# Kernel optimization log

Measured on AMD Instinct MI355X. Metric: run time of the kernel, lower is better.

Reference implementation:

```python
import jax, jax.numpy as jnp
import numpy as np

N, E, F, H, C, K = 50000, 1600000, 256, 6, 16, 40
NEG_SLOPE = 0.2  # PyG GATConv default
EPS = 1e-16


def _gat_layer(x, src, dst, W, a_s, a_d, b, heads, out_ch, concat):
    # linear transform per head: [N, heads, out_ch]
    h = (x @ W).reshape(N, heads, out_ch)
    # per-node attention logits
    al_s = jnp.einsum('nhc,hc->nh', h, a_s)  # source term
    al_d = jnp.einsum('nhc,hc->nh', h, a_d)  # destination term
    # edge-wise score + segment softmax over incoming edges of each dst node
    e = jax.nn.leaky_relu(al_s[src] + al_d[dst], NEG_SLOPE)  # [E', heads]
    m = jax.ops.segment_max(e, dst, num_segments=N)
    ex = jnp.exp(e - m[dst])
    denom = jax.ops.segment_sum(ex, dst, num_segments=N)
    alpha = ex / (denom[dst] + EPS)  # [E', heads]
    # weighted scatter-add aggregation
    out = jax.ops.segment_sum(h[src] * alpha[:, :, None], dst, num_segments=N)
    out = out.reshape(N, heads * out_ch) if concat else out.mean(axis=1)
    return out + b


def setup_inputs() -> dict:
    key = jax.random.key(0)
    ks = jax.random.split(key, 16)
    s = 0.05
    inp = {
        'x': jax.random.normal(ks[0], (N, F), dtype=jnp.float32),
        'edge_index': jax.random.randint(ks[1], (2, E), 0, N, dtype=jnp.int64 if jax.config.jax_enable_x64 else jnp.int32),
        'W1': jax.random.normal(ks[2], (F, H * C), dtype=jnp.float32) * s,
        'a1_s': jax.random.normal(ks[3], (H, C), dtype=jnp.float32) * s,
        'a1_d': jax.random.normal(ks[4], (H, C), dtype=jnp.float32) * s,
        'b1': jnp.zeros((H * C,), dtype=jnp.float32),
        'W2': jax.random.normal(ks[5], (H * C, H * C), dtype=jnp.float32) * s,
        'a2_s': jax.random.normal(ks[6], (H, C), dtype=jnp.float32) * s,
        'a2_d': jax.random.normal(ks[7], (H, C), dtype=jnp.float32) * s,
        'b2': jnp.zeros((H * C,), dtype=jnp.float32),
        'W3': jax.random.normal(ks[8], (H * C, H * C), dtype=jnp.float32) * s,
        'a3_s': jax.random.normal(ks[9], (H, C), dtype=jnp.float32) * s,
        'a3_d': jax.random.normal(ks[10], (H, C), dtype=jnp.float32) * s,
        'b3': jnp.zeros((H * C,), dtype=jnp.float32),
        'W4': jax.random.normal(ks[11], (H * C, K), dtype=jnp.float32) * s,
        'a4_s': jax.random.normal(ks[12], (1, K), dtype=jnp.float32) * s,
        'a4_d': jax.random.normal(ks[13], (1, K), dtype=jnp.float32) * s,
        'b4': jnp.zeros((K,), dtype=jnp.float32),
    }
    return inp


def reference(x, edge_index, W1, a1_s, a1_d, b1, W2, a2_s, a2_d, b2,
              W3, a3_s, a3_d, b3, W4, a4_s, a4_d, b4):
    # PyG GATConv adds self-loops by default
    loops = jnp.arange(N, dtype=edge_index.dtype)
    src = jnp.concatenate([edge_index[0], loops])
    dst = jnp.concatenate([edge_index[1], loops])
    # dropout is identity at eval time
    h = jax.nn.relu(_gat_layer(x, src, dst, W1, a1_s, a1_d, b1, H, C, True))
    h = jax.nn.relu(_gat_layer(h, src, dst, W2, a2_s, a2_d, b2, H, C, True))
    h = jax.nn.relu(_gat_layer(h, src, dst, W3, a3_s, a3_d, b3, H, C, True))
    h = _gat_layer(h, src, dst, W4, a4_s, a4_d, b4, 1, K, False)
    return jax.nn.log_softmax(h, axis=1)
```

## Files before the change

### kernel.cpp

```cpp
#include <hip/hip_runtime.h>
#include <cstdint>
#include <cstddef>

namespace {

constexpr int N  = 50000;
constexpr int E  = 1600000;
constexpr int ET = E + N;
constexpr int F  = 256;
constexpr int H  = 6;
constexpr int C  = 16;
constexpr int HC = H * C;
constexpr int K  = 40;
constexpr int NBUCK = (N + 255) / 256;
constexpr int EPB2  = 8192;
constexpr int HBLK  = (ET + EPB2 - 1) / EPB2;

typedef __attribute__((ext_vector_type(8))) short short8;
typedef __attribute__((ext_vector_type(4))) float f32x4;
typedef __attribute__((ext_vector_type(2))) float f32x2;

__device__ inline uint32_t f2bf(float f) {
  uint32_t u = __float_as_uint(f);
  return (u + 0x7FFFu + ((u >> 16) & 1u)) >> 16;
}
__device__ inline float bflo(uint32_t u) { return __uint_as_float(u << 16); }
__device__ inline float bfhi(uint32_t u) { return __uint_as_float(u & 0xFFFF0000u); }


__global__ void coarse_hist_kernel(const int* __restrict__ ei, int* __restrict__ hist) {
  __shared__ int h[256];
  const int t = threadIdx.x;
  h[t] = 0;
  __syncthreads();
  const int cbase = blockIdx.x * EPB2;
  const int cend = (cbase + EPB2 < ET) ? (cbase + EPB2) : ET;
  for (int e0 = cbase + t * 4; e0 < cend; e0 += 1024) {
    if (e0 + 3 < E && e0 + 3 < cend) {
      int4 dv = *reinterpret_cast<const int4*>(ei + E + e0);
      atomicAdd(&h[dv.x >> 8], 1);
      atomicAdd(&h[dv.y >> 8], 1);
      atomicAdd(&h[dv.z >> 8], 1);
      atomicAdd(&h[dv.w >> 8], 1);
    } else {
#pragma unroll
      for (int q = 0; q < 4; q++) {
        int e = e0 + q;
        if (e < cend) {
          int dd = (e < E) ? ei[E + e] : (e - E);
          atomicAdd(&h[dd >> 8], 1);
        }
      }
    }
  }
  __syncthreads();
  hist[blockIdx.x * 256 + t] = h[t];
}

__global__ void coarse_scan_kernel(const int* __restrict__ hist, int* __restrict__ base,
                                   int* __restrict__ bucket_base, int* __restrict__ rowp) {
  __shared__ int sc[256];
  const int d = threadIdx.x;
  int tot = 0;
#pragma unroll 4
  for (int b = 0; b < HBLK; b++) tot += hist[b * 256 + d];
  sc[d] = tot;
  __syncthreads();
  for (int off = 1; off < 256; off <<= 1) {
    int tv = (d >= off) ? sc[d - off] : 0;
    __syncthreads();
    sc[d] += tv;
    __syncthreads();
  }
  const int excl = sc[d] - tot;
  bucket_base[d] = excl;
  if (d == 255) {
    bucket_base[256] = sc[255];
    rowp[N] = sc[255];
  }
  int run = excl;
#pragma unroll 4
  for (int b = 0; b < HBLK; b++) {
    int v = hist[b * 256 + d];
    base[b * 256 + d] = run;
    run += v;
  }
}

__global__ void coarse_scatter_kernel(const int* __restrict__ ei, const int* __restrict__ base,
                                      uint32_t* __restrict__ keys) {
  __shared__ int cnt[256];
  const int t = threadIdx.x;
  cnt[t] = base[blockIdx.x * 256 + t];
  __syncthreads();
  const int cbase = blockIdx.x * EPB2;
  const int cend = (cbase + EPB2 < ET) ? (cbase + EPB2) : ET;
  for (int e0 = cbase + t * 4; e0 < cend; e0 += 1024) {
    if (e0 + 3 < E && e0 + 3 < cend) {
      int4 dv = *reinterpret_cast<const int4*>(ei + E + e0);
      int4 sv = *reinterpret_cast<const int4*>(ei + e0);
      int p0 = atomicAdd(&cnt[dv.x >> 8], 1);
      keys[p0] = ((uint32_t)dv.x << 16) | (uint32_t)sv.x;
      int p1 = atomicAdd(&cnt[dv.y >> 8], 1);
      keys[p1] = ((uint32_t)dv.y << 16) | (uint32_t)sv.y;
      int p2 = atomicAdd(&cnt[dv.z >> 8], 1);
      keys[p2] = ((uint32_t)dv.z << 16) | (uint32_t)sv.z;
      int p3 = atomicAdd(&cnt[dv.w >> 8], 1);
      keys[p3] = ((uint32_t)dv.w << 16) | (uint32_t)sv.w;
    } else {
#pragma unroll
      for (int q = 0; q < 4; q++) {
        int e = e0 + q;
        if (e < cend) {
          int dd, ssrc;
          if (e < E) { dd = ei[E + e]; ssrc = ei[e]; }
          else       { dd = e - E; ssrc = e - E; }
          int p = atomicAdd(&cnt[dd >> 8], 1);
          keys[p] = ((uint32_t)dd << 16) | (uint32_t)ssrc;
        }
      }
    }
  }
}

__global__ void bucket_sort_kernel(const uint32_t* __restrict__ keys,
                                   const int* __restrict__ bucket_base,
                                   int* __restrict__ rowp, int* __restrict__ col) {
  __shared__ int hist[256];
  __shared__ int sc[256];
  __shared__ int ofs[256];
  const int b = blockIdx.x;
  const int t = threadIdx.x;
  hist[t] = 0;
  __syncthreads();
  const int k0 = bucket_base[b], k1 = bucket_base[b + 1];
  for (int i = k0 + t; i < k1; i += 256)
    atomicAdd(&hist[(keys[i] >> 16) & 255], 1);
  __syncthreads();
  const int v = hist[t];
  sc[t] = v;
  __syncthreads();
  for (int off = 1; off < 256; off <<= 1) {
    int tv = (t >= off) ? sc[t - off] : 0;
    __syncthreads();
    sc[t] += tv;
    __syncthreads();
  }
  ofs[t] = k0 + sc[t] - v;
  const int node = b * 256 + t;
  if (node < N) rowp[node] = ofs[t];
  hist[t] = 0;
  __syncthreads();
  for (int i = k0 + t; i < k1; i += 256) {
    uint32_t key = keys[i];
    int loc = (key >> 16) & 255;
    int p = ofs[loc] + atomicAdd(&hist[loc], 1);
    col[p] = (int)(key & 0xFFFFu);
  }
}


__global__ void tobf16_kernel(const float* __restrict__ src, uint32_t* __restrict__ dst,
                              int n2) {
  int i = blockIdx.x * blockDim.x + threadIdx.x;
  if (i >= n2) return;
  float2 v = reinterpret_cast<const float2*>(src)[i];
  dst[i] = (f2bf(v.y) << 16) | f2bf(v.x);
}


__global__ void cvtW_kernel(const float* __restrict__ W1, const float* __restrict__ W2,
                            const float* __restrict__ W3, const float* __restrict__ W4,
                            uint16_t* __restrict__ WT1, uint16_t* __restrict__ WT2,
                            uint16_t* __restrict__ WT3, uint16_t* __restrict__ WT4) {
  constexpr int T1 = 96 * 256, T2 = 96 * 96, T3 = 96 * 96, T4 = 48 * 96;
  int t = blockIdx.x * blockDim.x + threadIdx.x;
  if (t < T1) {
    int n = t / 256, k = t % 256;
    WT1[t] = (uint16_t)f2bf(W1[(size_t)k * 96 + n]);
  } else if (t < T1 + T2) {
    int u = t - T1; int n = u / 96, k = u % 96;
    WT2[u] = (uint16_t)f2bf(W2[(size_t)k * 96 + n]);
  } else if (t < T1 + T2 + T3) {
    int u = t - T1 - T2; int n = u / 96, k = u % 96;
    WT3[u] = (uint16_t)f2bf(W3[(size_t)k * 96 + n]);
  } else if (t < T1 + T2 + T3 + T4) {
    int u = t - T1 - T2 - T3; int n = u / 96, k = u % 96;
    WT4[u] = (n < K) ? (uint16_t)f2bf(W4[(size_t)k * K + n]) : (uint16_t)0;
  }
}


template <int KD>
__launch_bounds__(256)
__global__ void gemm_pack_kernel(const uint32_t* __restrict__ A,
                                 const uint16_t* __restrict__ WT,
                                 const float* __restrict__ as_,
                                 const float* __restrict__ ad_,
                                 uint32_t* __restrict__ recs,
                                 float* __restrict__ aldP) {
  constexpr int KU = KD / 2;
  __shared__ float lds[64][97];
  const int wave = threadIdx.x >> 6;
  const int lane = threadIdx.x & 63;
  const int r = lane & 15, g = lane >> 4;
  const int m0 = (blockIdx.x * 4 + wave) * 16;
  int rowA = m0 + r;
  if (rowA > N - 1) rowA = N - 1;
  const uint32_t* arow = A + (size_t)rowA * KU + g * 4;
  const uint32_t* wt32 = reinterpret_cast<const uint32_t*>(WT);

  f32x4 acc[6];
#pragma unroll
  for (int nt = 0; nt < 6; nt++) acc[nt] = (f32x4){0.f, 0.f, 0.f, 0.f};

#pragma unroll
  for (int ks = 0; ks < KD / 32; ks++) {
    short8 av = *reinterpret_cast<const short8*>(arow + ks * 16);
#pragma unroll
    for (int nt = 0; nt < 6; nt++) {
      short8 bv = *reinterpret_cast<const short8*>(
          wt32 + (size_t)(nt * 16 + r) * KU + ks * 16 + g * 4);
      acc[nt] = __builtin_amdgcn_mfma_f32_16x16x32_bf16(av, bv, acc[nt], 0, 0, 0);
    }
  }

  const int lr0 = wave * 16 + g * 4;
#pragma unroll
  for (int nt = 0; nt < 6; nt++) {
#pragma unroll
    for (int t = 0; t < 4; t++) lds[lr0 + t][nt * 16 + r] = acc[nt][t];
  }
  __syncthreads();

  const int row = threadIdx.x >> 2;
  const int q = threadIdx.x & 3;
  const int grow = blockIdx.x * 64 + row;
  if (grow < N) {
    const float* lr = lds[row];
    uint32_t* rp = recs + (size_t)grow * 32;
#pragma unroll
    for (int w = 0; w < 6; w++) {
      const int c0 = q * 24 + w * 4;
      uint32_t wv = 0;
      wv = (uint32_t)__builtin_amdgcn_cvt_pk_fp8_f32(lr[c0], lr[c0 + 1], (int)wv, false);
      wv = (uint32_t)__builtin_amdgcn_cvt_pk_fp8_f32(lr[c0 + 2], lr[c0 + 3], (int)wv, true);
      rp[q * 6 + w] = wv;
    }
#pragma unroll
    for (int i = 0; i < 3; i++) {
      const int d = q * 3 + i;
      const int hh = d >> 1;
      const float* av = (d & 1) ? ad_ : as_;
      float s = 0.f;
#pragma unroll
      for (int c = 0; c < 16; c++) s += lr[hh * 16 + c] * av[hh * 16 + c];
      if (d & 1) aldP[(size_t)grow * 8 + hh] = s;
      else       rp[24 + hh] = __float_as_uint(s);
    }
  }
}


template <int KD, int NT, int NCOLS, int OST>
__launch_bounds__(256)
__global__ void mfma_gemm_kernel(const uint32_t* __restrict__ A,
                                 const uint16_t* __restrict__ WT,
                                 uint16_t* __restrict__ hOut, int M) {
  constexpr int KU = KD / 2;
  const int wave = threadIdx.x >> 6;
  const int lane = threadIdx.x & 63;
  const int m0 = (blockIdx.x * 4 + wave) * 16;
  if (m0 >= M) return;
  const int r = lane & 15, g = lane >> 4;
  int rowA = m0 + r;
  if (rowA > M - 1) rowA = M - 1;
  const uint32_t* arow = A + (size_t)rowA * KU + g * 4;
  const uint32_t* wt32 = reinterpret_cast<const uint32_t*>(WT);

  f32x4 acc[NT];
#pragma unroll
  for (int nt = 0; nt < NT; nt++) acc[nt] = (f32x4){0.f, 0.f, 0.f, 0.f};

#pragma unroll
  for (int ks = 0; ks < KD / 32; ks++) {
    short8 av = *reinterpret_cast<const short8*>(arow + ks * 16);
#pragma unroll
    for (int nt = 0; nt < NT; nt++) {
      short8 bv = *reinterpret_cast<const short8*>(
          wt32 + (size_t)(nt * 16 + r) * KU + ks * 16 + g * 4);
      acc[nt] = __builtin_amdgcn_mfma_f32_16x16x32_bf16(av, bv, acc[nt], 0, 0, 0);
    }
  }

  const int orow = m0 + g * 4;
#pragma unroll
  for (int nt = 0; nt < NT; nt++) {
    const int ocol = nt * 16 + r;
#pragma unroll
    for (int t = 0; t < 4; t++) {
      int rr = orow + t;
      if (rr < M && ocol < NCOLS)
        hOut[(size_t)rr * OST + ocol] = (uint16_t)f2bf(acc[nt][t]);
    }
  }
}


__global__ void pack4_kernel(const uint32_t* __restrict__ h4B,
                             const float* __restrict__ as_, const float* __restrict__ ad_,
                             uint32_t* __restrict__ recs4, float* __restrict__ ald4) {
  int n = blockIdx.x * 256 + threadIdx.x;
  if (n >= N) return;
  const uint32_t* hp = h4B + (size_t)n * 32;
  float f[40];
  float ss = 0.f, dd = 0.f;
#pragma unroll
  for (int i = 0; i < 20; i++) {
    uint32_t u = hp[i];
    f[2 * i] = bflo(u);
    f[2 * i + 1] = bfhi(u);
  }
#pragma unroll
  for (int c = 0; c < 40; c++) {
    ss += f[c] * as_[c];
    dd += f[c] * ad_[c];
  }
  uint32_t* rp = recs4 + (size_t)n * 16;
#pragma unroll
  for (int q = 0; q < 10; q++) {
    uint32_t w = 0;
    w = (uint32_t)__builtin_amdgcn_cvt_pk_fp8_f32(f[4 * q + 0], f[4 * q + 1], (int)w, false);
    w = (uint32_t)__builtin_amdgcn_cvt_pk_fp8_f32(f[4 * q + 2], f[4 * q + 3], (int)w, true);
    rp[q] = w;
  }
  rp[10] = __float_as_uint(ss);
  ald4[n] = dd;
}


template <int LPN, int NPW, int REC32, int ALSW, int HDIV, int PAD, bool LSM>
__launch_bounds__(256)
__global__ void flash_agg4_kernel(const uint32_t* __restrict__ recs,
                                  const int* __restrict__ rowp,
                                  const int* __restrict__ col,
                                  const float* __restrict__ aldP,
                                  const float* __restrict__ bias,
                                  uint4* __restrict__ outB4,
                                  float* __restrict__ outF32) {
  const int lane = threadIdx.x & 63;
  const int wave = threadIdx.x >> 6;
  int g = lane / LPN;
  const int li = lane - g * LPN;
  if (g > NPW - 1) g = NPW - 1;
  int n = (blockIdx.x * 4 + wave) * NPW + g;
  if (n > N - 1) n = N - 1;
  const int hh = li / HDIV;
  const float aldv = aldP[(size_t)n * PAD + hh];
  const int b0 = rowp[n];
  const int deg = rowp[n + 1] - b0;
  const int d1 = deg >> 1;
  const int d2 = deg - d1;

  int km = d2;
#pragma unroll
  for (int off = 32; off > 0; off >>= 1) {
    int o = __shfl_xor(km, off);
    km = (o > km) ? o : km;
  }

  float a0 = 0.f, a1 = 0.f, a2 = 0.f, a3 = 0.f;
  float a4 = 0.f, a5 = 0.f, a6 = 0.f, a7 = 0.f;
  float b0f = 0.f, b1f = 0.f, b2f = 0.f, b3f = 0.f;
  float b4f = 0.f, b5f = 0.f, b6f = 0.f, b7f = 0.f;
  float ssA = 0.f, ssB = 0.f;

  for (int k = 0; k < km; k++) {
    const bool vA = (k < d1);
    const bool vB = (k < d2);
    const int jA = b0 + (vA ? k : 0);
    const int jB = b0 + d1 + (vB ? k : 0);
    const int srcA = col[jA];
    const int srcB = col[jB];
    const uint32_t* recA = recs + (size_t)srcA * REC32;
    const uint32_t* recB = recs + (size_t)srcB * REC32;
    uint2 uA = *reinterpret_cast<const uint2*>(recA + 2 * li);
    uint2 uB = *reinterpret_cast<const uint2*>(recB + 2 * li);
    float lA = __uint_as_float(recA[ALSW + hh]);
    float lB = __uint_as_float(recB[ALSW + hh]);
    float eA = lA + aldv; eA = fmaxf(eA, 0.2f * eA);
    float eB = lB + aldv; eB = fmaxf(eB, 0.2f * eB);
    float pA = __expf(eA); pA = vA ? pA : 0.f;
    float pB = __expf(eB); pB = vB ? pB : 0.f;
    f32x2 cA0 = __builtin_amdgcn_cvt_pk_f32_fp8((int)uA.x, false);
    f32x2 cA1 = __builtin_amdgcn_cvt_pk_f32_fp8((int)uA.x, true);
    f32x2 cA2 = __builtin_amdgcn_cvt_pk_f32_fp8((int)uA.y, false);
    f32x2 cA3 = __builtin_amdgcn_cvt_pk_f32_fp8((int)uA.y, true);
    f32x2 cB0 = __builtin_amdgcn_cvt_pk_f32_fp8((int)uB.x, false);
    f32x2 cB1 = __builtin_amdgcn_cvt_pk_f32_fp8((int)uB.x, true);
    f32x2 cB2 = __builtin_amdgcn_cvt_pk_f32_fp8((int)uB.y, false);
    f32x2 cB3 = __builtin_amdgcn_cvt_pk_f32_fp8((int)uB.y, true);
    a0 += pA * cA0.x; a1 += pA * cA0.y;
    a2 += pA * cA1.x; a3 += pA * cA1.y;
    a4 += pA * cA2.x; a5 += pA * cA2.y;
    a6 += pA * cA3.x; a7 += pA * cA3.y;
    ssA += pA;
    b0f += pB * cB0.x; b1f += pB * cB0.y;
    b2f += pB * cB1.x; b3f += pB * cB1.y;
    b4f += pB * cB2.x; b5f += pB * cB2.y;
    b6f += pB * cB3.x; b7f += pB * cB3.y;
    ssB += pB;
  }

  a0 += b0f; a1 += b1f; a2 += b2f; a3 += b3f;
  a4 += b4f; a5 += b5f; a6 += b6f; a7 += b7f;
  float inv = 1.f / (ssA + ssB + 1e-16f);

  if (!LSM) {
    float o0 = fmaxf(a0 * inv + bias[8 * li + 0], 0.f);
    float o1 = fmaxf(a1 * inv + bias[8 * li + 1], 0.f);
    float o2 = fmaxf(a2 * inv + bias[8 * li + 2], 0.f);
    float o3 = fmaxf(a3 * inv + bias[8 * li + 3], 0.f);
    float o4 = fmaxf(a4 * inv + bias[8 * li + 4], 0.f);
    float o5 = fmaxf(a5 * inv + bias[8 * li + 5], 0.f);
    float o6 = fmaxf(a6 * inv + bias[8 * li + 6], 0.f);
    float o7 = fmaxf(a7 * inv + bias[8 * li + 7], 0.f);
    uint4 w;
    w.x = (f2bf(o1) << 16) | f2bf(o0);
    w.y = (f2bf(o3) << 16) | f2bf(o2);
    w.z = (f2bf(o5) << 16) | f2bf(o4);
    w.w = (f2bf(o7) << 16) | f2bf(o6);
    outB4[(size_t)n * LPN + li] = w;
  } else {
    bool vl = (li < 5);
    float v0 = vl ? a0 * inv + bias[8 * li + 0] : -1e30f;
    float v1 = vl ? a1 * inv + bias[8 * li + 1] : -1e30f;
    float v2 = vl ? a2 * inv + bias[8 * li + 2] : -1e30f;
    float v3 = vl ? a3 * inv + bias[8 * li + 3] : -1e30f;
    float v4 = vl ? a4 * inv + bias[8 * li + 4] : -1e30f;
    float v5 = vl ? a5 * inv + bias[8 * li + 5] : -1e30f;
    float v6 = vl ? a6 * inv + bias[8 * li + 6] : -1e30f;
    float v7 = vl ? a7 * inv + bias[8 * li + 7] : -1e30f;
    float mx = fmaxf(fmaxf(fmaxf(v0, v1), fmaxf(v2, v3)),
                     fmaxf(fmaxf(v4, v5), fmaxf(v6, v7)));
#pragma unroll
    for (int off = 1; off < 8; off <<= 1) mx = fmaxf(mx, __shfl_xor(mx, off));
    float es = 0.f;
    if (vl)
      es = __expf(v0 - mx) + __expf(v1 - mx) + __expf(v2 - mx) + __expf(v3 - mx) +
           __expf(v4 - mx) + __expf(v5 - mx) + __expf(v6 - mx) + __expf(v7 - mx);
#pragma unroll
    for (int off = 1; off < 8; off <<= 1) es += __shfl_xor(es, off);
    float lse = mx + __logf(es);
    if (vl) {
      float* op = outF32 + (size_t)n * K + li * 8;
      float4 w0 = make_float4(v0 - lse, v1 - lse, v2 - lse, v3 - lse);
      float4 w1 = make_float4(v4 - lse, v5 - lse, v6 - lse, v7 - lse);
      *reinterpret_cast<float4*>(op) = w0;
      *reinterpret_cast<float4*>(op + 4) = w1;
    }
  }
}

inline int cdiv(int a, int b) { return (a + b - 1) / b; }

}

extern "C" void kernel_launch(void* const* d_in, const int* in_sizes, int n_in,
                              void* d_out, int out_size, void* d_ws, size_t ws_size,
                              hipStream_t stream) {
  (void)in_sizes; (void)n_in; (void)out_size; (void)ws_size;
  const float* x   = (const float*)d_in[0];
  const int*   ei  = (const int*)d_in[1];
  const float* W1  = (const float*)d_in[2];
  const float* a1s = (const float*)d_in[3];
  const float* a1d = (const float*)d_in[4];
  const float* b1  = (const float*)d_in[5];
  const float* W2  = (const float*)d_in[6];
  const float* a2s = (const float*)d_in[7];
  const float* a2d = (const float*)d_in[8];
  const float* b2  = (const float*)d_in[9];
  const float* W3  = (const float*)d_in[10];
  const float* a3s = (const float*)d_in[11];
  const float* a3d = (const float*)d_in[12];
  const float* b3  = (const float*)d_in[13];
  const float* W4  = (const float*)d_in[14];
  const float* a4s = (const float*)d_in[15];
  const float* a4d = (const float*)d_in[16];
  const float* b4  = (const float*)d_in[17];
  float* out = (float*)d_out;

  char* ws = (char*)d_ws;
  size_t off = 0;
  auto alloc = [&](size_t bytes) {
    void* p = ws + off;
    off = (off + bytes + 255) & ~(size_t)255;
    return p;
  };
  int*      hist  = (int*)alloc((size_t)HBLK * 256 * 4);
  int*      basep = (int*)alloc((size_t)HBLK * 256 * 4);
  int*      bbase = (int*)alloc((size_t)257 * 4);
  int*      rowp  = (int*)alloc((size_t)(N + 1) * 4);
  uint32_t* keys  = (uint32_t*)alloc((size_t)ET * 4);
  int*      col   = (int*)alloc((size_t)ET * 4);
  uint32_t* xB    = (uint32_t*)alloc((size_t)N * (F / 2) * 4);
  uint16_t* WT1   = (uint16_t*)alloc((size_t)96 * 256 * 2);
  uint16_t* WT2   = (uint16_t*)alloc((size_t)96 * 96 * 2);
  uint16_t* WT3   = (uint16_t*)alloc((size_t)96 * 96 * 2);
  uint16_t* WT4   = (uint16_t*)alloc((size_t)48 * 96 * 2);
  uint32_t* actB  = (uint32_t*)alloc((size_t)N * (HC / 2) * 4);
  uint32_t* h4B   = (uint32_t*)alloc((size_t)N * 32 * 4);
  uint32_t* recs  = (uint32_t*)alloc((size_t)N * 32 * 4);
  uint32_t* recs4 = (uint32_t*)alloc((size_t)N * 16 * 4);
  float*    aldP  = (float*)alloc((size_t)N * 8 * 4);

  coarse_hist_kernel<<<HBLK, 256, 0, stream>>>(ei, hist);
  coarse_scan_kernel<<<1, 256, 0, stream>>>(hist, basep, bbase, rowp);
  coarse_scatter_kernel<<<HBLK, 256, 0, stream>>>(ei, basep, keys);
  bucket_sort_kernel<<<NBUCK, 256, 0, stream>>>(keys, bbase, rowp, col);

  tobf16_kernel<<<cdiv(N * (F / 2), 256), 256, 0, stream>>>(x, xB, N * (F / 2));
  cvtW_kernel<<<cdiv(96 * 256 + 96 * 96 * 2 + 48 * 96, 256), 256, 0, stream>>>(
      W1, W2, W3, W4, WT1, WT2, WT3, WT4);

  const int gN1  = cdiv(N, 256);
  const int gG   = cdiv(N, 64);
  const int gA96 = cdiv(N, 20);
  const int gA40 = cdiv(N, 32);

  gemm_pack_kernel<F><<<gG, 256, 0, stream>>>(xB, WT1, a1s, a1d, recs, aldP);
  flash_agg4_kernel<12, 5, 32, 24, 2, 8, false><<<gA96, 256, 0, stream>>>(
      recs, rowp, col, aldP, b1, (uint4*)actB, nullptr);

  gemm_pack_kernel<HC><<<gG, 256, 0, stream>>>(actB, WT2, a2s, a2d, recs, aldP);
  flash_agg4_kernel<12, 5, 32, 24, 2, 8, false><<<gA96, 256, 0, stream>>>(
      recs, rowp, col, aldP, b2, (uint4*)actB, nullptr);

  gemm_pack_kernel<HC><<<gG, 256, 0, stream>>>(actB, WT3, a3s, a3d, recs, aldP);
  flash_agg4_kernel<12, 5, 32, 24, 2, 8, false><<<gA96, 256, 0, stream>>>(
      recs, rowp, col, aldP, b3, (uint4*)actB, nullptr);

  mfma_gemm_kernel<HC, 3, K, 64><<<gG, 256, 0, stream>>>(actB, WT4, (uint16_t*)h4B, N);
  pack4_kernel<<<gN1, 256, 0, stream>>>(h4B, a4s, a4d, recs4, aldP);
  flash_agg4_kernel<8, 8, 16, 10, 16, 1, true><<<gA40, 256, 0, stream>>>(
      recs4, rowp, col, aldP, b4, nullptr, out);
}
```

Measured before the change: 308.5 us.

## Sort nodes by degree so aggregation waves process similar-degree nodes

Adds a counting sort of nodes by in-degree (histogram, scan, scatter kernels) producing a permutation, and the aggregation kernel now maps each lane group to perm[idx]. This is meant to cut intra-wave imbalance, where all node groups in a wave loop to the maximum degree. It also unrolls the edge loop by two. The costs are three extra small launches, and output writes and rowp reads become scattered rather than contiguous.

```diff
diff --git a/kernel.cpp b/kernel.cpp
--- a/kernel.cpp
+++ b/kernel.cpp
@@ -156,6 +156,60 @@
     int loc = (key >> 16) & 255;
     int p = ofs[loc] + atomicAdd(&hist[loc], 1);
     col[p] = (int)(key & 0xFFFFu);
+  }
+}
+
+
+__global__ void deg_hist_kernel(const int* __restrict__ rowp, int* __restrict__ dh) {
+  __shared__ int h[256];
+  const int t = threadIdx.x;
+  h[t] = 0;
+  __syncthreads();
+  int i = blockIdx.x * 256 + t;
+  if (i < N) {
+    int deg = rowp[i + 1] - rowp[i];
+    if (deg > 255) deg = 255;
+    atomicAdd(&h[deg], 1);
+  }
+  __syncthreads();
+  dh[blockIdx.x * 256 + t] = h[t];
+}
+
+__global__ void deg_scan_kernel(const int* __restrict__ dh, int* __restrict__ dbase) {
+  __shared__ int sc[256];
+  const int d = threadIdx.x;
+  int tot = 0;
+#pragma unroll 4
+  for (int b = 0; b < NBUCK; b++) tot += dh[b * 256 + d];
+  sc[d] = tot;
+  __syncthreads();
+  for (int off = 1; off < 256; off <<= 1) {
+    int tv = (d >= off) ? sc[d - off] : 0;
+    __syncthreads();
+    sc[d] += tv;
+    __syncthreads();
+  }
+  int run = sc[d] - tot;
+#pragma unroll 4
+  for (int b = 0; b < NBUCK; b++) {
+    int v = dh[b * 256 + d];
+    dbase[b * 256 + d] = run;
+    run += v;
+  }
+}
+
+__global__ void deg_scatter_kernel(const int* __restrict__ rowp, const int* __restrict__ dbase,
+                                   int* __restrict__ perm) {
+  __shared__ int cnt[256];
+  const int t = threadIdx.x;
+  cnt[t] = dbase[blockIdx.x * 256 + t];
+  __syncthreads();
+  int i = blockIdx.x * 256 + t;
+  if (i < N) {
+    int deg = rowp[i + 1] - rowp[i];
+    if (deg > 255) deg = 255;
+    int p = atomicAdd(&cnt[deg], 1);
+    perm[p] = i;
   }
 }
 
@@ -341,9 +395,10 @@
 
 template <int LPN, int NPW, int REC32, int ALSW, int HDIV, int PAD, bool LSM>
 __launch_bounds__(256)
-__global__ void flash_agg4_kernel(const uint32_t* __restrict__ recs,
+__global__ void flash_agg5_kernel(const uint32_t* __restrict__ recs,
                                   const int* __restrict__ rowp,
                                   const int* __restrict__ col,
+                                  const int* __restrict__ perm,
                                   const float* __restrict__ aldP,
                                   const float* __restrict__ bias,
                                   uint4* __restrict__ outB4,
@@ -353,8 +408,9 @@
   int g = lane / LPN;
   const int li = lane - g * LPN;
   if (g > NPW - 1) g = NPW - 1;
-  int n = (blockIdx.x * 4 + wave) * NPW + g;
-  if (n > N - 1) n = N - 1;
+  int idx = (blockIdx.x * 4 + wave) * NPW + g;
+  if (idx > N - 1) idx = N - 1;
+  const int n = perm[idx];
   const int hh = li / HDIV;
   const float aldv = aldP[(size_t)n * PAD + hh];
   const int b0 = rowp[n];
@@ -375,6 +431,7 @@
   float b4f = 0.f, b5f = 0.f, b6f = 0.f, b7f = 0.f;
   float ssA = 0.f, ssB = 0.f;
 
+#pragma unroll 2
   for (int k = 0; k < km; k++) {
     const bool vA = (k < d1);
     const bool vB = (k < d2);
@@ -503,6 +560,7 @@
   int*      rowp  = (int*)alloc((size_t)(N + 1) * 4);
   uint32_t* keys  = (uint32_t*)alloc((size_t)ET * 4);
   int*      col   = (int*)alloc((size_t)ET * 4);
+  int*      perm  = (int*)alloc((size_t)N * 4);
   uint32_t* xB    = (uint32_t*)alloc((size_t)N * (F / 2) * 4);
   uint16_t* WT1   = (uint16_t*)alloc((size_t)96 * 256 * 2);
   uint16_t* WT2   = (uint16_t*)alloc((size_t)96 * 96 * 2);
@@ -519,6 +577,10 @@
   coarse_scatter_kernel<<<HBLK, 256, 0, stream>>>(ei, basep, keys);
   bucket_sort_kernel<<<NBUCK, 256, 0, stream>>>(keys, bbase, rowp, col);
 
+  deg_hist_kernel<<<NBUCK, 256, 0, stream>>>(rowp, hist);
+  deg_scan_kernel<<<1, 256, 0, stream>>>(hist, basep);
+  deg_scatter_kernel<<<NBUCK, 256, 0, stream>>>(rowp, basep, perm);
+
   tobf16_kernel<<<cdiv(N * (F / 2), 256), 256, 0, stream>>>(x, xB, N * (F / 2));
   cvtW_kernel<<<cdiv(96 * 256 + 96 * 96 * 2 + 48 * 96, 256), 256, 0, stream>>>(
       W1, W2, W3, W4, WT1, WT2, WT3, WT4);
@@ -529,19 +591,19 @@
   const int gA40 = cdiv(N, 32);
 
   gemm_pack_kernel<F><<<gG, 256, 0, stream>>>(xB, WT1, a1s, a1d, recs, aldP);
-  flash_agg4_kernel<12, 5, 32, 24, 2, 8, false><<<gA96, 256, 0, stream>>>(
-      recs, rowp, col, aldP, b1, (uint4*)actB, nullptr);
+  flash_agg5_kernel<12, 5, 32, 24, 2, 8, false><<<gA96, 256, 0, stream>>>(
+      recs, rowp, col, perm, aldP, b1, (uint4*)actB, nullptr);
 
   gemm_pack_kernel<HC><<<gG, 256, 0, stream>>>(actB, WT2, a2s, a2d, recs, aldP);
-  flash_agg4_kernel<12, 5, 32, 24, 2, 8, false><<<gA96, 256, 0, stream>>>(
-      recs, rowp, col, aldP, b2, (uint4*)actB, nullptr);
+  flash_agg5_kernel<12, 5, 32, 24, 2, 8, false><<<gA96, 256, 0, stream>>>(
+      recs, rowp, col, perm, aldP, b2, (uint4*)actB, nullptr);
 
   gemm_pack_kernel<HC><<<gG, 256, 0, stream>>>(actB, WT3, a3s, a3d, recs, aldP);
-  flash_agg4_kernel<12, 5, 32, 24, 2, 8, false><<<gA96, 256, 0, stream>>>(
-      recs, rowp, col, aldP, b3, (uint4*)actB, nullptr);
+  flash_agg5_kernel<12, 5, 32, 24, 2, 8, false><<<gA96, 256, 0, stream>>>(
+      recs, rowp, col, perm, aldP, b3, (uint4*)actB, nullptr);
 
   mfma_gemm_kernel<HC, 3, K, 64><<<gG, 256, 0, stream>>>(actB, WT4, (uint16_t*)h4B, N);
   pack4_kernel<<<gN1, 256, 0, stream>>>(h4B, a4s, a4d, recs4, aldP);
-  flash_agg4_kernel<8, 8, 16, 10, 16, 1, true><<<gA40, 256, 0, stream>>>(
-      recs4, rowp, col, aldP, b4, nullptr, out);
-}
+  flash_agg5_kernel<8, 8, 16, 10, 16, 1, true><<<gA40, 256, 0, stream>>>(
+      recs4, rowp, col, perm, aldP, b4, nullptr, out);
+}
```

Measured after the change: 309.3 us. About the same (+0.3%).
